# Performance work log

Hardware: AMD Instinct MI355X
Metric: run time of the kernel (lower is better)

The kernel has to match this reference:

```python
import jax, jax.numpy as jnp
import numpy as np

# module hyper-parameters (from init_kwargs)
IN_H, IN_W = 64, 44
OUT_H, OUT_W = 48, 22
DT_OFF, DX_OFF, DY_OFF = 0.5, 0.5, 0.5
SIGMA_OFF, DELTA_OFF = 1.0, 1.0
EPS = 1e-8
K_PO = 2  # ProgressiveOffset k


def _progressive_offset(v, k=K_PO):
    # torch: x += detach(x) shifted right by i with zero fill, scaled 1/k, for i=1..k
    vd = jax.lax.stop_gradient(v)
    out = v
    T = v.shape[1]
    for i in range(1, k + 1):
        out = out + jnp.pad(vd, ((0, 0), (i, 0)))[:, :T] * (1.0 / k)
    return out


def setup_inputs() -> dict:
    key = jax.random.key(0)
    ks = jax.random.split(key, 9)
    N, C, T = 16, 64, 30
    return {
        "x": jax.random.normal(ks[0], (N, C, T, IN_H, IN_W), jnp.float32),
        "dx": jax.random.normal(ks[1], (N, T), jnp.float32),
        "dy": jax.random.normal(ks[2], (N, T), jnp.float32),
        "log_sigma2": jax.random.normal(ks[3], (N, T), jnp.float32),
        "log_delta": jax.random.normal(ks[4], (N, T), jnp.float32),
        "log_gamma": jax.random.normal(ks[5], (N, T), jnp.float32),
        "dt": jax.random.normal(ks[6], (N,), jnp.float32),
        "log_delta_t": jax.random.normal(ks[7], (N,), jnp.float32),
        "log_gamma_t": jax.random.normal(ks[8], (N,), jnp.float32),
    }


def reference(x, dx, dy, log_sigma2, log_delta, log_gamma, dt, log_delta_t, log_gamma_t):
    N, C, T, H, W = x.shape
    NT = N * T
    a_w = OUT_W
    a_h = int(round(OUT_W / IN_W * IN_H))  # attended spatial height (32)

    anchor_t = T * DT_OFF
    anchor_x = W * DX_OFF
    anchor_y = H * DY_OFF

    # --- localization params ---
    dxv = jnp.tanh(_progressive_offset(dx).reshape(NT, 1)) * (IN_W / 2.0) + anchor_x
    dyv = jnp.tanh(_progressive_offset(dy).reshape(NT, 1)) * (IN_H / 2.0) + anchor_y
    sigma2 = jnp.exp(log_sigma2).reshape(NT, 1) * SIGMA_OFF
    delta = jnp.exp(log_delta).reshape(NT, 1) * DELTA_OFF
    gamma = jax.nn.sigmoid(log_gamma).reshape(NT)
    dtv = jnp.tanh(dt) * (T / 2.0) + anchor_t           # (N,)
    delta_t = jnp.exp(log_delta_t) * DELTA_OFF          # (N,)
    gamma_t = jax.nn.sigmoid(log_gamma_t)               # (N,)

    # --- Gaussian spatial filter banks ---
    gx = jnp.arange(a_w, dtype=x.dtype)
    gy = jnp.arange(a_h, dtype=x.dtype)
    mu_x = dxv + (gx[None, :] - a_w / 2.0) * delta      # (NT, a_w)
    mu_y = dyv + (gy[None, :] - a_h / 2.0) * delta      # (NT, a_h)
    a = jnp.arange(W, dtype=x.dtype)[None, None, :]
    b = jnp.arange(H, dtype=x.dtype)[None, None, :]
    s2 = sigma2[:, :, None]                              # (NT,1,1)
    Fx = jnp.exp(-((a - mu_x[:, :, None]) ** 2) / (2.0 * s2))  # (NT, a_w, W)
    Fy = jnp.exp(-((b - mu_y[:, :, None]) ** 2) / (2.0 * s2))  # (NT, a_h, H)
    Fx = Fx / jnp.maximum(jnp.sum(Fx, axis=2, keepdims=True), EPS)
    Fy = Fy / jnp.maximum(jnp.sum(Fy, axis=2, keepdims=True), EPS)

    # --- spatial glimpse: Fy @ x @ Fx^T, batched over (N*T, C) ---
    xf = jnp.transpose(x, (0, 2, 1, 3, 4)).reshape(NT, C, H, W)
    glimpse = jnp.einsum('nih,nchw,njw->ncij', Fy, xf, Fx)  # (NT, C, a_h, a_w)
    glimpse = glimpse * gamma[:, None, None, None]

    # --- temporal transform (grid_sample, align_corners=False, zero padding) ---
    gt = jnp.arange(T, dtype=x.dtype)
    mu_t = dtv[:, None] + (gt[None, :] - T / 2.0) * delta_t[:, None]  # (N, T)
    mu_t = mu_t / (T - 1) * 2.0 - 1.0
    # y-axis sample coords in input index space
    iy = ((mu_t + 1.0) * T - 1.0) / 2.0
    iy0 = jnp.floor(iy)
    w1 = iy - iy0
    w0 = 1.0 - w1
    i0 = iy0.astype(jnp.int32)
    i1 = i0 + 1
    v0 = ((i0 >= 0) & (i0 < T)).astype(x.dtype)
    v1 = ((i1 >= 0) & (i1 < T)).astype(x.dtype)
    g = glimpse.reshape(N, T, C * a_h * a_w)             # (N, T, Chw)
    g0 = jnp.take_along_axis(g, jnp.clip(i0, 0, T - 1)[:, :, None], axis=1)
    g1 = jnp.take_along_axis(g, jnp.clip(i1, 0, T - 1)[:, :, None], axis=1)
    # x-grid coord is fixed at -1 with width-1 input -> factor 0.5 (half in zero pad)
    out_t = 0.5 * ((w0 * v0)[:, :, None] * g0 + (w1 * v1)[:, :, None] * g1)

    out = out_t.reshape(N, T, C, a_h, a_w).transpose(0, 2, 1, 3, 4)  # (N,C,T,a_h,a_w)
    out = out * gamma_t[:, None, None, None, None]

    pad_t = (OUT_H - a_h) // 2
    pad_b = OUT_H - pad_t - a_h
    out = jnp.pad(out, ((0, 0), (0, 0), (0, 0), (pad_t, pad_b), (0, 0)))
    return out
```

## Files before the change

### kernel.cpp

```cpp
#include <hip/hip_runtime.h>
#include <math.h>


#define EPS_ 1e-8f

__global__ __launch_bounds__(256) void gst_kernel(
    const float* __restrict__ x,
    const float* __restrict__ dx,  const float* __restrict__ dy,
    const float* __restrict__ ls2, const float* __restrict__ ld,
    const float* __restrict__ lg,
    const float* __restrict__ dtp, const float* __restrict__ ldt,
    const float* __restrict__ lgt,
    float* __restrict__ out)
{
    __shared__ float FyT[64][36];
    __shared__ float FxT[44][24];
    __shared__ float t2s[8][64][24];

    const int tid = threadIdx.x;
    int b = blockIdx.x;
    const int cg = b & 7; b >>= 3;
    const int tq = b % 30;
    const int n  = b / 30;

    const float dtv     = tanhf(dtp[n]) * 15.f + 15.f;
    const float delta_t = expf(ldt[n]);
    const float gamma_t = 1.f / (1.f + expf(-lgt[n]));
    float mu_t = dtv + ((float)tq - 15.f) * delta_t;
    mu_t = mu_t / 29.f * 2.f - 1.f;
    const float iy  = ((mu_t + 1.f) * 30.f - 1.f) * 0.5f;
    const float iy0 = floorf(iy);
    const float w1  = iy - iy0;
    const int   i0  = (int)iy0;
    const int   i1  = i0 + 1;
    const float W0 = (i0 >= 0 && i0 < 30) ? 0.5f * gamma_t * (1.f - w1) : 0.f;
    const float W1 = (i1 >= 0 && i1 < 30) ? 0.5f * gamma_t * w1 : 0.f;
    const int t0 = min(max(i0, 0), 29);
    const int t1 = min(max(i1, 0), 29);

    const int c_loc = tid >> 5;
    const int hp    = tid & 31;
    const int jt    = tid & 3;
    const int it    = (tid >> 2) & 7;
    const int j0    = 6 * jt;
    const int i0r   = 4 * it;

    float acc2[4][6];
#pragma unroll
    for (int r = 0; r < 4; ++r)
#pragma unroll
        for (int s2 = 0; s2 < 6; ++s2) acc2[r][s2] = 0.f;

#pragma unroll 1
    for (int s = 0; s < 2; ++s) {
        const float Ws = s ? W1 : W0;
        const int   ts = s ? t1 : t0;
        if (Ws == 0.f) continue;

        __syncthreads();

        {
            const int nt = n * 30 + ts;
            const float sigma2 = expf(ls2[nt]);
            const float inv2s2 = 0.5f / sigma2;
            const float delta  = expf(ld[nt]);
            const float gamma  = 1.f / (1.f + expf(-lg[nt]));
            const float A      = Ws * gamma;
            if (tid < 32) {
                float pod = dy[nt] + 0.5f * (ts >= 1 ? dy[nt - 1] : 0.f)
                                   + 0.5f * (ts >= 2 ? dy[nt - 2] : 0.f);
                const float muy = tanhf(pod) * 32.f + 32.f;
                const float mu  = muy + ((float)tid - 16.f) * delta;
                float sum = 0.f;
                for (int h = 0; h < 64; ++h) {
                    float d = (float)h - mu; sum += expf(-d * d * inv2s2);
                }
                const float sc = A / fmaxf(sum, EPS_);
                for (int h = 0; h < 64; ++h) {
                    float d = (float)h - mu;
                    FyT[h][tid] = expf(-d * d * inv2s2) * sc;
                }
            } else if (tid < 54) {
                const int j = tid - 32;
                float pod = dx[nt] + 0.5f * (ts >= 1 ? dx[nt - 1] : 0.f)
                                   + 0.5f * (ts >= 2 ? dx[nt - 2] : 0.f);
                const float mux = tanhf(pod) * 22.f + 22.f;
                const float mu  = mux + ((float)j - 11.f) * delta;
                float sum = 0.f;
                for (int w = 0; w < 44; ++w) {
                    float d = (float)w - mu; sum += expf(-d * d * inv2s2);
                }
                const float sc = 1.f / fmaxf(sum, EPS_);
                for (int w = 0; w < 44; ++w) {
                    float d = (float)w - mu;
                    FxT[w][j] = expf(-d * d * inv2s2) * sc;
                }
            }
        }
        __syncthreads();

        {
            float a0[22], a1[22];
#pragma unroll
            for (int j = 0; j < 22; ++j) { a0[j] = 0.f; a1[j] = 0.f; }

            const size_t xoff =
                ((((size_t)n * 64 + (size_t)(cg * 8 + c_loc)) * 30 + (size_t)ts) * 64
                 + (size_t)(2 * hp)) * 44;
            const float4* xr0 = reinterpret_cast<const float4*>(x + xoff);
            const float4* xr1 = reinterpret_cast<const float4*>(x + xoff + 44);

#pragma unroll 2
            for (int wi = 0; wi < 11; ++wi) {
                const float4 xa = xr0[wi];
                const float4 xb = xr1[wi];
                const float xav[4] = { xa.x, xa.y, xa.z, xa.w };
                const float xbv[4] = { xb.x, xb.y, xb.z, xb.w };
#pragma unroll
                for (int k = 0; k < 4; ++k) {
                    const float4* fxr =
                        reinterpret_cast<const float4*>(&FxT[4 * wi + k][0]);
                    const float4 f0 = fxr[0], f1 = fxr[1], f2 = fxr[2],
                                 f3 = fxr[3], f4 = fxr[4];
                    const float2 f5 =
                        *reinterpret_cast<const float2*>(&FxT[4 * wi + k][20]);
                    const float fv[22] = { f0.x, f0.y, f0.z, f0.w,
                                           f1.x, f1.y, f1.z, f1.w,
                                           f2.x, f2.y, f2.z, f2.w,
                                           f3.x, f3.y, f3.z, f3.w,
                                           f4.x, f4.y, f4.z, f4.w,
                                           f5.x, f5.y };
                    const float va = xav[k], vb = xbv[k];
#pragma unroll
                    for (int j = 0; j < 22; ++j) {
                        a0[j] += va * fv[j];
                        a1[j] += vb * fv[j];
                    }
                }
            }
            float4* d0 = reinterpret_cast<float4*>(&t2s[c_loc][2 * hp][0]);
            float4* d1 = reinterpret_cast<float4*>(&t2s[c_loc][2 * hp + 1][0]);
            d0[0] = make_float4(a0[0],  a0[1],  a0[2],  a0[3]);
            d0[1] = make_float4(a0[4],  a0[5],  a0[6],  a0[7]);
            d0[2] = make_float4(a0[8],  a0[9],  a0[10], a0[11]);
            d0[3] = make_float4(a0[12], a0[13], a0[14], a0[15]);
            d0[4] = make_float4(a0[16], a0[17], a0[18], a0[19]);
            d0[5] = make_float4(a0[20], a0[21], 0.f, 0.f);
            d1[0] = make_float4(a1[0],  a1[1],  a1[2],  a1[3]);
            d1[1] = make_float4(a1[4],  a1[5],  a1[6],  a1[7]);
            d1[2] = make_float4(a1[8],  a1[9],  a1[10], a1[11]);
            d1[3] = make_float4(a1[12], a1[13], a1[14], a1[15]);
            d1[4] = make_float4(a1[16], a1[17], a1[18], a1[19]);
            d1[5] = make_float4(a1[20], a1[21], 0.f, 0.f);
        }
        __syncthreads();

        {
#pragma unroll 2
            for (int h4 = 0; h4 < 16; ++h4) {
#pragma unroll
                for (int k = 0; k < 4; ++k) {
                    const int h = 4 * h4 + k;
                    const float4 fy =
                        *reinterpret_cast<const float4*>(&FyT[h][i0r]);
                    const float2* tp =
                        reinterpret_cast<const float2*>(&t2s[c_loc][h][j0]);
                    const float2 q0 = tp[0], q1 = tp[1], q2 = tp[2];
                    const float fyv[4] = { fy.x, fy.y, fy.z, fy.w };
                    const float tv[6]  = { q0.x, q0.y, q1.x, q1.y, q2.x, q2.y };
#pragma unroll
                    for (int r = 0; r < 4; ++r)
#pragma unroll
                        for (int s2 = 0; s2 < 6; ++s2)
                            acc2[r][s2] += fyv[r] * tv[s2];
                }
            }
        }
    }

    const size_t ob =
        (((size_t)n * 64 + (size_t)(cg * 8)) * 30 + (size_t)tq) * 1056;

    for (int idx = tid; idx < 8 * 16 * 22; idx += 256) {
        const int c   = idx / 352;
        const int rem = idx % 352;
        const int r   = rem / 22;
        const int j   = rem % 22;
        const int ip  = (r < 8) ? r : (r + 32);
        out[ob + (size_t)c * 31680 + (size_t)(ip * 22 + j)] = 0.f;
    }

#pragma unroll
    for (int r = 0; r < 4; ++r) {
#pragma unroll
        for (int s2 = 0; s2 < 6; ++s2) {
            const int j = j0 + s2;
            if (j < 22) {
                out[ob + (size_t)c_loc * 31680
                       + (size_t)((8 + i0r + r) * 22 + j)] = acc2[r][s2];
            }
        }
    }
}

extern "C" void kernel_launch(void* const* d_in, const int* in_sizes, int n_in,
                              void* d_out, int out_size, void* d_ws, size_t ws_size,
                              hipStream_t stream) {
    const float* x   = (const float*)d_in[0];
    const float* dx  = (const float*)d_in[1];
    const float* dy  = (const float*)d_in[2];
    const float* ls2 = (const float*)d_in[3];
    const float* ld  = (const float*)d_in[4];
    const float* lg  = (const float*)d_in[5];
    const float* dtp = (const float*)d_in[6];
    const float* ldt = (const float*)d_in[7];
    const float* lgt = (const float*)d_in[8];
    float* out = (float*)d_out;

    dim3 grid(16 * 30 * 8), block(256);
    hipLaunchKernelGGL(gst_kernel, grid, block, 0, stream,
                       x, dx, dy, ls2, ld, lg, dtp, ldt, lgt, out);
}
```

Measured before the change: 683.4 us.

## Halve shared staging buffer, split H into two chunks, parallelize filter-bank build

Shrinks the intermediate shared buffer to 32 rows and processes the 64 input rows in two passes with one row per thread. This cuts register pressure (a single 22-wide accumulator) and LDS use, with launch_bounds asking for 4 blocks per SM. The Gaussian filter-bank construction is now spread over all 256 threads, four lanes per filter combined with shuffles, instead of 54 threads running serial 64- and 44-long loops. The trade-off is extra barriers per time step and less ILP per thread, and each thread now issues 11 float4 loads up front.

```diff
diff --git a/kernel.cpp b/kernel.cpp
--- a/kernel.cpp
+++ b/kernel.cpp
@@ -4,7 +4,7 @@
 
 #define EPS_ 1e-8f
 
-__global__ __launch_bounds__(256) void gst_kernel(
+__global__ __launch_bounds__(256, 4) void gst_kernel(
     const float* __restrict__ x,
     const float* __restrict__ dx,  const float* __restrict__ dy,
     const float* __restrict__ ls2, const float* __restrict__ ld,
@@ -15,7 +15,7 @@
 {
     __shared__ float FyT[64][36];
     __shared__ float FxT[44][24];
-    __shared__ float t2s[8][64][24];
+    __shared__ float t2s[8][32][24];
 
     const int tid = threadIdx.x;
     int b = blockIdx.x;
@@ -51,120 +51,120 @@
 #pragma unroll
         for (int s2 = 0; s2 < 6; ++s2) acc2[r][s2] = 0.f;
 
+    bool first = true;
 #pragma unroll 1
     for (int s = 0; s < 2; ++s) {
         const float Ws = s ? W1 : W0;
         const int   ts = s ? t1 : t0;
         if (Ws == 0.f) continue;
-
-        __syncthreads();
-
-        {
-            const int nt = n * 30 + ts;
-            const float sigma2 = expf(ls2[nt]);
-            const float inv2s2 = 0.5f / sigma2;
-            const float delta  = expf(ld[nt]);
-            const float gamma  = 1.f / (1.f + expf(-lg[nt]));
-            const float A      = Ws * gamma;
-            if (tid < 32) {
-                float pod = dy[nt] + 0.5f * (ts >= 1 ? dy[nt - 1] : 0.f)
-                                   + 0.5f * (ts >= 2 ? dy[nt - 2] : 0.f);
-                const float muy = tanhf(pod) * 32.f + 32.f;
-                const float mu  = muy + ((float)tid - 16.f) * delta;
-                float sum = 0.f;
-                for (int h = 0; h < 64; ++h) {
-                    float d = (float)h - mu; sum += expf(-d * d * inv2s2);
-                }
-                const float sc = A / fmaxf(sum, EPS_);
-                for (int h = 0; h < 64; ++h) {
-                    float d = (float)h - mu;
-                    FyT[h][tid] = expf(-d * d * inv2s2) * sc;
-                }
-            } else if (tid < 54) {
-                const int j = tid - 32;
-                float pod = dx[nt] + 0.5f * (ts >= 1 ? dx[nt - 1] : 0.f)
-                                   + 0.5f * (ts >= 2 ? dx[nt - 2] : 0.f);
-                const float mux = tanhf(pod) * 22.f + 22.f;
-                const float mu  = mux + ((float)j - 11.f) * delta;
-                float sum = 0.f;
-                for (int w = 0; w < 44; ++w) {
-                    float d = (float)w - mu; sum += expf(-d * d * inv2s2);
-                }
-                const float sc = 1.f / fmaxf(sum, EPS_);
-                for (int w = 0; w < 44; ++w) {
-                    float d = (float)w - mu;
-                    FxT[w][j] = expf(-d * d * inv2s2) * sc;
-                }
+        if (!first) __syncthreads();
+        first = false;
+
+        const int nt = n * 30 + ts;
+        const float sigma2 = expf(ls2[nt]);
+        const float inv2s2 = 0.5f / sigma2;
+        const float delta  = expf(ld[nt]);
+        const float gamma  = 1.f / (1.f + expf(-lg[nt]));
+        const float A      = Ws * gamma;
+
+        if (tid < 128) {
+            const int i = tid >> 2, q = tid & 3;
+            float pod = dy[nt] + 0.5f * (ts >= 1 ? dy[nt - 1] : 0.f)
+                               + 0.5f * (ts >= 2 ? dy[nt - 2] : 0.f);
+            const float mu = tanhf(pod) * 32.f + 32.f + ((float)i - 16.f) * delta;
+            float e[16];
+            float sum = 0.f;
+#pragma unroll
+            for (int k = 0; k < 16; ++k) {
+                const float d = (float)(16 * q + k) - mu;
+                e[k] = expf(-d * d * inv2s2);
+                sum += e[k];
+            }
+            sum += __shfl_xor(sum, 1);
+            sum += __shfl_xor(sum, 2);
+            const float sc = A / fmaxf(sum, EPS_);
+#pragma unroll
+            for (int k = 0; k < 16; ++k)
+                FyT[16 * q + k][i] = e[k] * sc;
+        } else {
+            const int tx = tid - 128;
+            const int j = tx >> 2, q = tx & 3;
+            float pod = dx[nt] + 0.5f * (ts >= 1 ? dx[nt - 1] : 0.f)
+                               + 0.5f * (ts >= 2 ? dx[nt - 2] : 0.f);
+            const float mu = tanhf(pod) * 22.f + 22.f + ((float)j - 11.f) * delta;
+            float e[11];
+            float sum = 0.f;
+#pragma unroll
+            for (int m = 0; m < 11; ++m) {
+                const float d = (float)(11 * q + m) - mu;
+                e[m] = expf(-d * d * inv2s2);
+                sum += e[m];
+            }
+            sum += __shfl_xor(sum, 1);
+            sum += __shfl_xor(sum, 2);
+            const float sc = 1.f / fmaxf(sum, EPS_);
+            if (j < 22) {
+#pragma unroll
+                for (int m = 0; m < 11; ++m)
+                    FxT[11 * q + m][j] = e[m] * sc;
             }
         }
         __syncthreads();
 
-        {
-            float a0[22], a1[22];
-#pragma unroll
-            for (int j = 0; j < 22; ++j) { a0[j] = 0.f; a1[j] = 0.f; }
-
-            const size_t xoff =
-                ((((size_t)n * 64 + (size_t)(cg * 8 + c_loc)) * 30 + (size_t)ts) * 64
-                 + (size_t)(2 * hp)) * 44;
-            const float4* xr0 = reinterpret_cast<const float4*>(x + xoff);
-            const float4* xr1 = reinterpret_cast<const float4*>(x + xoff + 44);
-
-#pragma unroll 2
-            for (int wi = 0; wi < 11; ++wi) {
-                const float4 xa = xr0[wi];
-                const float4 xb = xr1[wi];
-                const float xav[4] = { xa.x, xa.y, xa.z, xa.w };
-                const float xbv[4] = { xb.x, xb.y, xb.z, xb.w };
-#pragma unroll
-                for (int k = 0; k < 4; ++k) {
-                    const float4* fxr =
-                        reinterpret_cast<const float4*>(&FxT[4 * wi + k][0]);
-                    const float4 f0 = fxr[0], f1 = fxr[1], f2 = fxr[2],
-                                 f3 = fxr[3], f4 = fxr[4];
-                    const float2 f5 =
-                        *reinterpret_cast<const float2*>(&FxT[4 * wi + k][20]);
-                    const float fv[22] = { f0.x, f0.y, f0.z, f0.w,
-                                           f1.x, f1.y, f1.z, f1.w,
-                                           f2.x, f2.y, f2.z, f2.w,
-                                           f3.x, f3.y, f3.z, f3.w,
-                                           f4.x, f4.y, f4.z, f4.w,
-                                           f5.x, f5.y };
-                    const float va = xav[k], vb = xbv[k];
-#pragma unroll
-                    for (int j = 0; j < 22; ++j) {
-                        a0[j] += va * fv[j];
-                        a1[j] += vb * fv[j];
+#pragma unroll 1
+        for (int hc = 0; hc < 2; ++hc) {
+            {
+                const size_t xoff =
+                    ((((size_t)n * 64 + (size_t)(cg * 8 + c_loc)) * 30
+                      + (size_t)ts) * 64 + (size_t)(32 * hc + hp)) * 44;
+                const float4* xr = reinterpret_cast<const float4*>(x + xoff);
+                float4 xv[11];
+#pragma unroll
+                for (int wi = 0; wi < 11; ++wi) xv[wi] = xr[wi];
+
+                float a0[22];
+#pragma unroll
+                for (int j = 0; j < 22; ++j) a0[j] = 0.f;
+
+#pragma unroll
+                for (int wi = 0; wi < 11; ++wi) {
+                    const float xav[4] = { xv[wi].x, xv[wi].y, xv[wi].z, xv[wi].w };
+#pragma unroll
+                    for (int k = 0; k < 4; ++k) {
+                        const float4* fxr =
+                            reinterpret_cast<const float4*>(&FxT[4 * wi + k][0]);
+                        const float4 f0 = fxr[0], f1 = fxr[1], f2 = fxr[2],
+                                     f3 = fxr[3], f4 = fxr[4];
+                        const float2 f5 =
+                            *reinterpret_cast<const float2*>(&FxT[4 * wi + k][20]);
+                        const float fv[22] = { f0.x, f0.y, f0.z, f0.w,
+                                               f1.x, f1.y, f1.z, f1.w,
+                                               f2.x, f2.y, f2.z, f2.w,
+                                               f3.x, f3.y, f3.z, f3.w,
+                                               f4.x, f4.y, f4.z, f4.w,
+                                               f5.x, f5.y };
+                        const float va = xav[k];
+#pragma unroll
+                        for (int j = 0; j < 22; ++j) a0[j] += va * fv[j];
                     }
                 }
-            }
-            float4* d0 = reinterpret_cast<float4*>(&t2s[c_loc][2 * hp][0]);
-            float4* d1 = reinterpret_cast<float4*>(&t2s[c_loc][2 * hp + 1][0]);
-            d0[0] = make_float4(a0[0],  a0[1],  a0[2],  a0[3]);
-            d0[1] = make_float4(a0[4],  a0[5],  a0[6],  a0[7]);
-            d0[2] = make_float4(a0[8],  a0[9],  a0[10], a0[11]);
-            d0[3] = make_float4(a0[12], a0[13], a0[14], a0[15]);
-            d0[4] = make_float4(a0[16], a0[17], a0[18], a0[19]);
-            d0[5] = make_float4(a0[20], a0[21], 0.f, 0.f);
-            d1[0] = make_float4(a1[0],  a1[1],  a1[2],  a1[3]);
-            d1[1] = make_float4(a1[4],  a1[5],  a1[6],  a1[7]);
-            d1[2] = make_float4(a1[8],  a1[9],  a1[10], a1[11]);
-            d1[3] = make_float4(a1[12], a1[13], a1[14], a1[15]);
-            d1[4] = make_float4(a1[16], a1[17], a1[18], a1[19]);
-            d1[5] = make_float4(a1[20], a1[21], 0.f, 0.f);
-        }
-        __syncthreads();
-
-        {
-#pragma unroll 2
-            for (int h4 = 0; h4 < 16; ++h4) {
-#pragma unroll
-                for (int k = 0; k < 4; ++k) {
-                    const int h = 4 * h4 + k;
+                float4* d0 = reinterpret_cast<float4*>(&t2s[c_loc][hp][0]);
+                d0[0] = make_float4(a0[0],  a0[1],  a0[2],  a0[3]);
+                d0[1] = make_float4(a0[4],  a0[5],  a0[6],  a0[7]);
+                d0[2] = make_float4(a0[8],  a0[9],  a0[10], a0[11]);
+                d0[3] = make_float4(a0[12], a0[13], a0[14], a0[15]);
+                d0[4] = make_float4(a0[16], a0[17], a0[18], a0[19]);
+                d0[5] = make_float4(a0[20], a0[21], 0.f, 0.f);
+            }
+            __syncthreads();
+
+            {
+#pragma unroll 4
+                for (int hp2 = 0; hp2 < 32; ++hp2) {
                     const float4 fy =
-                        *reinterpret_cast<const float4*>(&FyT[h][i0r]);
+                        *reinterpret_cast<const float4*>(&FyT[32 * hc + hp2][i0r]);
                     const float2* tp =
-                        reinterpret_cast<const float2*>(&t2s[c_loc][h][j0]);
+                        reinterpret_cast<const float2*>(&t2s[c_loc][hp2][j0]);
                     const float2 q0 = tp[0], q1 = tp[1], q2 = tp[2];
                     const float fyv[4] = { fy.x, fy.y, fy.z, fy.w };
                     const float tv[6]  = { q0.x, q0.y, q1.x, q1.y, q2.x, q2.y };
@@ -175,6 +175,7 @@
                             acc2[r][s2] += fyv[r] * tv[s2];
                 }
             }
+            if (hc == 0) __syncthreads();
         }
     }
 
```

New measurement: 787.3 us. +15.2%, slower.
